# Optimization experiments

Hardware: AMD Instinct MI355X
Metric: run time of the kernel (lower is better)

Reference implementation:

```python
import jax, jax.numpy as jnp
import numpy as np

CUTOFF = 5.0
EMB = 64
RAD = 32
N_ATOMS = 20000
N_SPECIES = 100
N_EDGES = 200000


def setup_inputs() -> dict:
    key = jax.random.key(0)
    k = jax.random.split(key, 8)
    Z = jax.random.randint(k[0], (N_ATOMS,), 0, N_SPECIES)
    neighbour_index = jax.random.randint(k[1], (N_EDGES, 2), 0, N_ATOMS)
    # random 3D offsets; norm ~1.6 << cutoff so envelope is active
    neighbour_vectors = jax.random.normal(k[2], (N_EDGES, 3), dtype=jnp.float32)
    z_embed = jax.random.normal(k[3], (N_SPECIES, EMB), dtype=jnp.float32) * 0.1
    z_map_w = jax.random.normal(k[4], (EMB, 2 * EMB), dtype=jnp.float32) / np.sqrt(2 * EMB)
    r_map_w = jax.random.normal(k[5], (3 * EMB, RAD), dtype=jnp.float32) / np.sqrt(RAD)
    r_map_b = jax.random.normal(k[6], (3 * EMB,), dtype=jnp.float32) * 0.01
    # PhysNet-style exponential RBF: centers in (exp(-cutoff), 1], fixed width
    rbf_centers = jnp.linspace(np.exp(-CUTOFF), 1.0, RAD, dtype=jnp.float32)
    beta_val = ((2.0 / RAD) * (1.0 - np.exp(-CUTOFF))) ** -2
    rbf_betas = jnp.full((RAD,), beta_val, dtype=jnp.float32)
    return {
        "Z": Z,
        "neighbour_index": neighbour_index,
        "neighbour_vectors": neighbour_vectors,
        "z_embed": z_embed,
        "z_map_w": z_map_w,
        "r_map_w": r_map_w,
        "r_map_b": r_map_b,
        "rbf_centers": rbf_centers,
        "rbf_betas": rbf_betas,
    }


def _edge_embedding(Z, neighbour_index, neighbour_vectors, z_embed,
                    z_map_w, r_map_w, r_map_b, rbf_centers, rbf_betas):
    r = jnp.linalg.norm(neighbour_vectors, axis=-1)          # [E]
    r_hat = neighbour_vectors / r[:, None]                   # [E,3]

    # initial geometric tensors
    x, y, z = r_hat[:, 0], r_hat[:, 1], r_hat[:, 2]
    zero = jnp.zeros_like(x)
    A0 = jnp.stack([zero, -z, y,
                    z, zero, -x,
                    -y, x, zero], axis=1).reshape(-1, 3, 3)   # [E,3,3] skew
    outer = r_hat[:, :, None] * r_hat[:, None, :]             # [E,3,3]
    tr_mean = (outer[:, 0, 0] + outer[:, 1, 1] + outer[:, 2, 2]) / 3.0
    eye3 = jnp.eye(3, dtype=neighbour_vectors.dtype)
    S0 = outer - tr_mean[:, None, None] * eye3                # symmetric, traceless

    # species embedding per edge: concat(embed(z_i) || embed(z_j)) -> linear (no bias)
    h_z_atom = z_embed[Z]                                     # [N,emb]
    h_z_edge = h_z_atom[neighbour_index].reshape(-1, 2 * EMB)  # [E,2emb]
    h_z_edge = h_z_edge @ z_map_w.T                           # [E,emb]

    # exponential radial basis + cosine envelope
    expansion = jnp.exp(-rbf_betas * (jnp.exp(-r)[:, None] - rbf_centers) ** 2)  # [E,rad]
    env = jnp.where(r < CUTOFF, 0.5 * (jnp.cos(jnp.pi * r / CUTOFF) + 1.0), 0.0)  # [E]

    c = (expansion @ r_map_w.T + r_map_b) * env[:, None] * jnp.tile(h_z_edge, (1, 3))  # [E,3emb]
    c_I, c_A, c_S = jnp.split(c, 3, axis=1)                   # each [E,emb]

    out_I = c_I[:, :, None, None] * eye3                       # [E,emb,3,3]
    out_A = c_A[:, :, None, None] * A0[:, None, :, :]
    out_S = c_S[:, :, None, None] * S0[:, None, :, :]
    return out_I, out_A, out_S


def reference(Z, neighbour_index, neighbour_vectors, z_embed,
              z_map_w, r_map_w, r_map_b, rbf_centers, rbf_betas):
    return _edge_embedding(Z, neighbour_index, neighbour_vectors, z_embed,
                           z_map_w, r_map_w, r_map_b, rbf_centers, rbf_betas)
```

## Files before the change

kernel.cpp:

```cpp
#include <hip/hip_runtime.h>

#define EMB 64
#define RAD 32
#define CUTOFF_F 5.0f

typedef float f32x4 __attribute__((ext_vector_type(4)));

__global__ void species_proj_kernel(const float* __restrict__ z_embed,
                                    const float* __restrict__ z_map_w,
                                    float* __restrict__ pA,
                                    float* __restrict__ pB) {
    const int s = blockIdx.x;
    const int k = threadIdx.x;
    const float* ze = z_embed + s * EMB;
    const float* wk = z_map_w + k * (2 * EMB);
    float a = 0.f, b = 0.f;
#pragma unroll 8
    for (int j = 0; j < EMB; ++j) {
        const float e = ze[j];
        a = fmaf(e, wk[j], a);
        b = fmaf(e, wk[EMB + j], b);
    }
    pA[s * EMB + k] = a;
    pB[s * EMB + k] = b;
}

__global__ __launch_bounds__(256) void edge_embed_kernel(
    const int* __restrict__ Z,
    const int* __restrict__ nbr,
    const float* __restrict__ nv,
    const float* __restrict__ rmw,
    const float* __restrict__ rmb,
    const float* __restrict__ rbfc,
    const float* __restrict__ rbfb,
    const float* __restrict__ pA,
    const float* __restrict__ pB,
    float* __restrict__ out,
    int E) {
    __shared__ __align__(16) float buf[4][3 * EMB * 9];

    const int tid  = threadIdx.x;
    const int w    = tid >> 6;
    const int lane = tid & 63;

    float W0[RAD], W1[RAD], W2[RAD];
#pragma unroll
    for (int j = 0; j < RAD; ++j) {
        W0[j] = rmw[lane * RAD + j];
        W1[j] = rmw[(lane + EMB) * RAD + j];
        W2[j] = rmw[(lane + 2 * EMB) * RAD + j];
    }
    const float b0 = rmb[lane], b1 = rmb[lane + EMB], b2 = rmb[lane + 2 * EMB];
    const float cj = rbfc[lane & (RAD - 1)];
    const float bj = rbfb[lane & (RAD - 1)];

    float* bw = buf[w];
    {
        const int o = lane * 9;
        bw[o + 1] = 0.f; bw[o + 2] = 0.f; bw[o + 3] = 0.f;
        bw[o + 5] = 0.f; bw[o + 6] = 0.f; bw[o + 7] = 0.f;
        bw[576 + o + 0] = 0.f; bw[576 + o + 4] = 0.f; bw[576 + o + 8] = 0.f;
    }

    const size_t strideT = (size_t)E * (EMB * 9);
    const int nw = gridDim.x * 4;
    int e = __builtin_amdgcn_readfirstlane(blockIdx.x * 4 + w);
    if (e >= E) return;

    int   i0 = nbr[2 * e], i1 = nbr[2 * e + 1];
    float vx = nv[3 * e], vy = nv[3 * e + 1], vz = nv[3 * e + 2];
    int   s0 = Z[i0], s1 = Z[i1];
    float hA = pA[s0 * EMB + lane], hB = pB[s1 * EMB + lane];

    while (true) {
        const int  en   = __builtin_amdgcn_readfirstlane(e + nw);
        const bool more = en < E;

        int ni0 = 0, ni1 = 0;
        float nvx = 0.f, nvy = 0.f, nvz = 0.f;
        if (more) {
            ni0 = nbr[2 * en]; ni1 = nbr[2 * en + 1];
            nvx = nv[3 * en]; nvy = nv[3 * en + 1]; nvz = nv[3 * en + 2];
        }

        const float r2   = vx * vx + vy * vy + vz * vz;
        const float rinv = rsqrtf(r2);
        const float r    = r2 * rinv;
        const float x = vx * rinv, y = vy * rinv, z = vz * rinv;

        float env = 0.f;
        if (r < CUTOFF_F)
            env = 0.5f * (__cosf(0.6283185307f * r) + 1.0f);

        const float t = __expf(-r);
        const float d = t - cj;
        const float g = __expf(-bj * d * d);

        int ns0 = 0, ns1 = 0;
        if (more) { ns0 = Z[ni0]; ns1 = Z[ni1]; }

        float aI = b0, aA = b1, aS = b2;
#pragma unroll
        for (int j = 0; j < RAD; ++j) {
            const float gj =
                __int_as_float(__builtin_amdgcn_readlane(__float_as_int(g), j));
            aI = fmaf(gj, W0[j], aI);
            aA = fmaf(gj, W1[j], aA);
            aS = fmaf(gj, W2[j], aS);
        }

        float nhA = 0.f, nhB = 0.f;
        if (more) { nhA = pA[ns0 * EMB + lane]; nhB = pB[ns1 * EMB + lane]; }

        const float eh = env * (hA + hB);
        const float cI = aI * eh, cA = aA * eh, cS = aS * eh;

        const int o = lane * 9;
        bw[o + 0] = cI; bw[o + 4] = cI; bw[o + 8] = cI;

        bw[576 + o + 1] = -z * cA; bw[576 + o + 2] =  y * cA;
        bw[576 + o + 3] =  z * cA; bw[576 + o + 5] = -x * cA;
        bw[576 + o + 6] = -y * cA; bw[576 + o + 7] =  x * cA;

        const float m = (x * x + y * y + z * z) * (1.f / 3.f);
        bw[1152 + o + 0] = (x * x - m) * cS;
        bw[1152 + o + 1] = x * y * cS;
        bw[1152 + o + 2] = x * z * cS;
        bw[1152 + o + 3] = x * y * cS;
        bw[1152 + o + 4] = (y * y - m) * cS;
        bw[1152 + o + 5] = y * z * cS;
        bw[1152 + o + 6] = x * z * cS;
        bw[1152 + o + 7] = y * z * cS;
        bw[1152 + o + 8] = (z * z - m) * cS;

        const size_t ebase = (size_t)e * (EMB * 9);
#pragma unroll
        for (int ts = 0; ts < 3; ++ts) {
#pragma unroll
            for (int i = 0; i < 3; ++i) {
                const int q = lane + (i << 6);
                if (q < 144) {
                    const f32x4 v =
                        *reinterpret_cast<const f32x4*>(bw + ts * 576 + 4 * q);
                    *reinterpret_cast<f32x4*>(out + strideT * ts + ebase + 4 * q) = v;
                }
            }
        }

        if (!more) break;
        e = en;
        vx = nvx; vy = nvy; vz = nvz;
        hA = nhA; hB = nhB;
    }
}

extern "C" void kernel_launch(void* const* d_in, const int* in_sizes, int n_in,
                              void* d_out, int out_size, void* d_ws, size_t ws_size,
                              hipStream_t stream) {
    const int*   Z       = (const int*)d_in[0];
    const int*   nbr     = (const int*)d_in[1];
    const float* nv      = (const float*)d_in[2];
    const float* z_embed = (const float*)d_in[3];
    const float* z_map_w = (const float*)d_in[4];
    const float* rmw     = (const float*)d_in[5];
    const float* rmb     = (const float*)d_in[6];
    const float* rbfc    = (const float*)d_in[7];
    const float* rbfb    = (const float*)d_in[8];
    float*       out     = (float*)d_out;

    const int E         = in_sizes[2] / 3;
    const int n_species = in_sizes[3] / EMB;

    float* pA = (float*)d_ws;
    float* pB = pA + (size_t)n_species * EMB;

    species_proj_kernel<<<n_species, EMB, 0, stream>>>(z_embed, z_map_w, pA, pB);
    edge_embed_kernel<<<2000, 256, 0, stream>>>(Z, nbr, nv, rmw, rmb, rbfc, rbfb,
                                                pA, pB, out, E);
}
```

Before: 279.6 us.

## Split edge work across three waves, one per output tensor type

Each wavefront now handles a single output tensor (I, A or S) for its edges instead of all three. This cuts per-wave register use for the weights from three rows to one and shrinks the shared staging buffer threefold, raising occupancy. The grid is tripled so there are enough waves to cover the extra split. In exchange, the per-edge geometry, RBF, and species gathers are recomputed three times, once by each wave that handles that edge.

```diff
diff --git a/kernel.cpp b/kernel.cpp
--- a/kernel.cpp
+++ b/kernel.cpp
@@ -37,34 +37,36 @@
     const float* __restrict__ pB,
     float* __restrict__ out,
     int E) {
-    __shared__ __align__(16) float buf[4][3 * EMB * 9];
+    __shared__ __align__(16) float buf[4][EMB * 9];
 
     const int tid  = threadIdx.x;
     const int w    = tid >> 6;
     const int lane = tid & 63;
 
-    float W0[RAD], W1[RAD], W2[RAD];
+    const int gw  = blockIdx.x * 4 + w;
+    const int t   = gw % 3;
+    const int nwT = (gridDim.x * 4) / 3;
+
+    const int row = lane + t * EMB;
+    float W[RAD];
 #pragma unroll
-    for (int j = 0; j < RAD; ++j) {
-        W0[j] = rmw[lane * RAD + j];
-        W1[j] = rmw[(lane + EMB) * RAD + j];
-        W2[j] = rmw[(lane + 2 * EMB) * RAD + j];
-    }
-    const float b0 = rmb[lane], b1 = rmb[lane + EMB], b2 = rmb[lane + 2 * EMB];
+    for (int j = 0; j < RAD; ++j) W[j] = rmw[row * RAD + j];
+    const float bb = rmb[row];
     const float cj = rbfc[lane & (RAD - 1)];
     const float bj = rbfb[lane & (RAD - 1)];
 
     float* bw = buf[w];
-    {
-        const int o = lane * 9;
+    const int o = lane * 9;
+    if (t == 0) {
         bw[o + 1] = 0.f; bw[o + 2] = 0.f; bw[o + 3] = 0.f;
         bw[o + 5] = 0.f; bw[o + 6] = 0.f; bw[o + 7] = 0.f;
-        bw[576 + o + 0] = 0.f; bw[576 + o + 4] = 0.f; bw[576 + o + 8] = 0.f;
+    } else if (t == 1) {
+        bw[o + 0] = 0.f; bw[o + 4] = 0.f; bw[o + 8] = 0.f;
     }
 
-    const size_t strideT = (size_t)E * (EMB * 9);
-    const int nw = gridDim.x * 4;
-    int e = __builtin_amdgcn_readfirstlane(blockIdx.x * 4 + w);
+    float* __restrict__ outT = out + (size_t)t * E * (EMB * 9);
+
+    int e = __builtin_amdgcn_readfirstlane(gw / 3);
     if (e >= E) return;
 
     int   i0 = nbr[2 * e], i1 = nbr[2 * e + 1];
@@ -73,7 +75,7 @@
     float hA = pA[s0 * EMB + lane], hB = pB[s1 * EMB + lane];
 
     while (true) {
-        const int  en   = __builtin_amdgcn_readfirstlane(e + nw);
+        const int  en   = __builtin_amdgcn_readfirstlane(e + nwT);
         const bool more = en < E;
 
         int ni0 = 0, ni1 = 0;
@@ -92,58 +94,54 @@
         if (r < CUTOFF_F)
             env = 0.5f * (__cosf(0.6283185307f * r) + 1.0f);
 
-        const float t = __expf(-r);
-        const float d = t - cj;
-        const float g = __expf(-bj * d * d);
+        const float ex = __expf(-r);
+        const float d  = ex - cj;
+        const float g  = __expf(-bj * d * d);
 
         int ns0 = 0, ns1 = 0;
         if (more) { ns0 = Z[ni0]; ns1 = Z[ni1]; }
 
-        float aI = b0, aA = b1, aS = b2;
+        float a = bb;
 #pragma unroll
         for (int j = 0; j < RAD; ++j) {
             const float gj =
                 __int_as_float(__builtin_amdgcn_readlane(__float_as_int(g), j));
-            aI = fmaf(gj, W0[j], aI);
-            aA = fmaf(gj, W1[j], aA);
-            aS = fmaf(gj, W2[j], aS);
+            a = fmaf(gj, W[j], a);
         }
 
         float nhA = 0.f, nhB = 0.f;
         if (more) { nhA = pA[ns0 * EMB + lane]; nhB = pB[ns1 * EMB + lane]; }
 
-        const float eh = env * (hA + hB);
-        const float cI = aI * eh, cA = aA * eh, cS = aS * eh;
+        const float c = a * env * (hA + hB);
 
-        const int o = lane * 9;
-        bw[o + 0] = cI; bw[o + 4] = cI; bw[o + 8] = cI;
-
-        bw[576 + o + 1] = -z * cA; bw[576 + o + 2] =  y * cA;
-        bw[576 + o + 3] =  z * cA; bw[576 + o + 5] = -x * cA;
-        bw[576 + o + 6] = -y * cA; bw[576 + o + 7] =  x * cA;
-
-        const float m = (x * x + y * y + z * z) * (1.f / 3.f);
-        bw[1152 + o + 0] = (x * x - m) * cS;
-        bw[1152 + o + 1] = x * y * cS;
-        bw[1152 + o + 2] = x * z * cS;
-        bw[1152 + o + 3] = x * y * cS;
-        bw[1152 + o + 4] = (y * y - m) * cS;
-        bw[1152 + o + 5] = y * z * cS;
-        bw[1152 + o + 6] = x * z * cS;
-        bw[1152 + o + 7] = y * z * cS;
-        bw[1152 + o + 8] = (z * z - m) * cS;
+        if (t == 0) {
+            bw[o + 0] = c; bw[o + 4] = c; bw[o + 8] = c;
+        } else if (t == 1) {
+            bw[o + 1] = -z * c; bw[o + 2] =  y * c;
+            bw[o + 3] =  z * c; bw[o + 5] = -x * c;
+            bw[o + 6] = -y * c; bw[o + 7] =  x * c;
+        } else {
+            const float m = (x * x + y * y + z * z) * (1.f / 3.f);
+            bw[o + 0] = (x * x - m) * c;
+            bw[o + 1] = x * y * c;
+            bw[o + 2] = x * z * c;
+            bw[o + 3] = x * y * c;
+            bw[o + 4] = (y * y - m) * c;
+            bw[o + 5] = y * z * c;
+            bw[o + 6] = x * z * c;
+            bw[o + 7] = y * z * c;
+            bw[o + 8] = (z * z - m) * c;
+        }
 
         const size_t ebase = (size_t)e * (EMB * 9);
-#pragma unroll
-        for (int ts = 0; ts < 3; ++ts) {
-#pragma unroll
-            for (int i = 0; i < 3; ++i) {
-                const int q = lane + (i << 6);
-                if (q < 144) {
-                    const f32x4 v =
-                        *reinterpret_cast<const f32x4*>(bw + ts * 576 + 4 * q);
-                    *reinterpret_cast<f32x4*>(out + strideT * ts + ebase + 4 * q) = v;
-                }
+        {
+            const f32x4 v0 = *reinterpret_cast<const f32x4*>(bw + 4 * lane);
+            *reinterpret_cast<f32x4*>(outT + ebase + 4 * lane) = v0;
+            const f32x4 v1 = *reinterpret_cast<const f32x4*>(bw + 4 * (lane + 64));
+            *reinterpret_cast<f32x4*>(outT + ebase + 4 * (lane + 64)) = v1;
+            if (lane < 16) {
+                const f32x4 v2 = *reinterpret_cast<const f32x4*>(bw + 4 * (lane + 128));
+                *reinterpret_cast<f32x4*>(outT + ebase + 4 * (lane + 128)) = v2;
             }
         }
 
@@ -175,6 +173,6 @@
     float* pB = pA + (size_t)n_species * EMB;
 
     species_proj_kernel<<<n_species, EMB, 0, stream>>>(z_embed, z_map_w, pA, pB);
-    edge_embed_kernel<<<2000, 256, 0, stream>>>(Z, nbr, nv, rmw, rmb, rbfc, rbfb,
+    edge_embed_kernel<<<6000, 256, 0, stream>>>(Z, nbr, nv, rmw, rmb, rbfc, rbfb,
                                                 pA, pB, out, E);
 }
```

Result: no change. 281.1 us (+0.6%).
